# Performance work log

Hardware: AMD Instinct MI355X
Metric: run time of the kernel (lower is better)

Reference implementation:

```python
import jax, jax.numpy as jnp
import numpy as np

S = 2        # scale
KUP = 5      # k_up
EPS = 1e-5   # BatchNorm eps


def _conv(x, w, p):
    return jax.lax.conv_general_dilated(
        x, w, (1, 1), [(p, p), (p, p)],
        dimension_numbers=('NCHW', 'OIHW', 'NCHW'))


def _bn(x, g, b, m, v):
    sc = g * jax.lax.rsqrt(v + EPS)
    return x * sc[None, :, None, None] + (b - m * sc)[None, :, None, None]


def setup_inputs() -> dict:
    key = jax.random.key(0)
    ks = jax.random.split(key, 11)
    c, c_mid = 256, 64
    return {
        'X': jax.random.normal(ks[0], (2, c, 48, 48), jnp.float32),
        'w_comp': jax.random.normal(ks[1], (c_mid, c, 1, 1), jnp.float32) * 0.05,
        'g1': jax.random.uniform(ks[2], (c_mid,), jnp.float32, 0.5, 1.5),
        'b1': jax.random.normal(ks[3], (c_mid,), jnp.float32) * 0.1,
        'm1': jax.random.normal(ks[4], (c_mid,), jnp.float32) * 0.1,
        'v1': jax.random.uniform(ks[5], (c_mid,), jnp.float32, 0.5, 1.5),
        'w_enc': jax.random.normal(ks[6], (100, c_mid, 3, 3), jnp.float32) * 0.05,
        'g2': jax.random.uniform(ks[7], (100,), jnp.float32, 0.5, 1.5),
        'b2': jax.random.normal(ks[8], (100,), jnp.float32) * 0.1,
        'm2': jax.random.normal(ks[9], (100,), jnp.float32) * 0.1,
        'v2': jax.random.uniform(ks[10], (100,), jnp.float32, 0.5, 1.5),
    }


def reference(X, w_comp, g1, b1, m1, v1, w_enc, g2, b2, m2, v2):
    b, c, h, w = X.shape
    h_, w_ = h * S, w * S
    k2 = KUP * KUP
    # comp: 1x1 conv + BN + SiLU
    t = _bn(_conv(X, w_comp, 0), g1, b1, m1, v1)
    t = t * jax.nn.sigmoid(t)
    # enc: 3x3 conv + BN (no act) -> (b, (S*KUP)^2, h, w)
    e = _bn(_conv(t, w_enc, 1), g2, b2, m2, v2)
    # PixelShuffle(S): (b, k2*S*S, h, w) -> (b, k2, h*S, w*S)
    e = e.reshape(b, k2, S, S, h, w).transpose(0, 1, 4, 2, 5, 3).reshape(b, k2, h_, w_)
    Wk = jax.nn.softmax(e, axis=1)  # per-pixel reassembly weights over k_up^2 taps
    # nearest-neighbor upsample by S
    Xup = jnp.repeat(jnp.repeat(X, S, axis=2), S, axis=3)
    # Unfold(kernel=KUP, dilation=S, padding=(KUP//2)*S): spatial size preserved
    pad = (KUP // 2) * S
    xp = jnp.pad(Xup, ((0, 0), (0, 0), (pad, pad), (pad, pad)))
    # taps in row-major (ky, kx) order, matching torch Unfold + view(b,c,k2,h_,w_)
    patches = jnp.stack(
        [xp[:, :, i * S:i * S + h_, j * S:j * S + w_]
         for i in range(KUP) for j in range(KUP)], axis=2)  # (b, c, k2, h_, w_)
    return jnp.einsum('bkhw,bckhw->bchw', Wk, patches)
```

## Files before the change

### kernel.cpp

```cpp
#include <hip/hip_runtime.h>

#define EPS_BN 1e-5f

typedef __attribute__((ext_vector_type(8))) short short8v;
typedef __attribute__((ext_vector_type(4))) float f32x4;
typedef __attribute__((ext_vector_type(4))) _Float16 h16x4;

__device__ inline unsigned short f2bf(float f) {
    union { float f; unsigned u; } v; v.f = f;
    unsigned r = v.u + 0x7fffu + ((v.u >> 16) & 1u);
    return (unsigned short)(r >> 16);
}

__global__ __launch_bounds__(256) void comp_mfma(
    const float* __restrict__ X, const float* __restrict__ w_comp,
    const float* __restrict__ w_enc,
    const float* __restrict__ g1, const float* __restrict__ b1,
    const float* __restrict__ m1, const float* __restrict__ v1,
    unsigned short* __restrict__ tpad, unsigned short* __restrict__ Web)
{
    const int wseg = blockIdx.x;
    const int h = blockIdx.y;
    const int b = blockIdx.z;
    const int tid  = threadIdx.x;

    {
        const int i = ((wseg + 3*(h + 48*b)) << 8) | tid;
        const int ch = i / 576;
        const int r  = i - ch * 576;
        const int kk = r >> 6;
        const int ci = r & 63;
        const float v = (ch < 100) ? w_enc[ch * 576 + ci * 9 + kk] : 0.f;
        Web[i] = f2bf(v);
        if (i < 25088) {
            const int bb  = i / 12544;
            const int rem = i - bb * 12544;
            const int p   = rem >> 6;
            const int chn = rem & 63;
            int rr, cc;
            if (p < 50)       { rr = 0;       cc = p;       }
            else if (p < 100) { rr = 49;      cc = p - 50;  }
            else if (p < 148) { rr = p - 99;  cc = 0;       }
            else              { rr = p - 147; cc = 49;      }
            tpad[((bb*50 + rr)*50 + cc)*64 + chn] = 0;
        }
    }

    const int wave = tid >> 6;
    const int l    = tid & 63;
    const int lr   = l & 15;
    const int lk   = l >> 4;
    const int w0   = wseg * 16;

    const float* xb = X + (size_t)b * 589824 + h * 48 + w0 + lr;
    const float* wb = w_comp + (wave * 16 + lr) * 256;

    float xpre[64];
    #pragma unroll
    for (int s = 0; s < 8; ++s)
        #pragma unroll
        for (int j = 0; j < 8; ++j)
            xpre[s*8 + j] = xb[(size_t)(s*32 + lk*8 + j) * 2304];

    f32x4 acc = {0.f,0.f,0.f,0.f};
    #pragma unroll
    for (int s = 0; s < 8; ++s) {
        const int ci0 = s * 32 + lk * 8;
        short8v a, f;
        const float4 wv0 = *(const float4*)(wb + ci0);
        const float4 wv1 = *(const float4*)(wb + ci0 + 4);
        f[0] = (short)f2bf(wv0.x); f[1] = (short)f2bf(wv0.y);
        f[2] = (short)f2bf(wv0.z); f[3] = (short)f2bf(wv0.w);
        f[4] = (short)f2bf(wv1.x); f[5] = (short)f2bf(wv1.y);
        f[6] = (short)f2bf(wv1.z); f[7] = (short)f2bf(wv1.w);
        #pragma unroll
        for (int j = 0; j < 8; ++j)
            a[j] = (short)f2bf(xpre[s*8 + j]);
        acc = __builtin_amdgcn_mfma_f32_16x16x32_bf16(a, f, acc, 0, 0, 0);
    }

    const int oc = wave * 16 + lr;
    const float sc = g1[oc] * rsqrtf(v1[oc] + EPS_BN);
    const float sh = b1[oc] - m1[oc] * sc;
    unsigned short* tp = tpad + ((b*50 + h + 1)*50 + 1)*64 + oc;
    #pragma unroll
    for (int r = 0; r < 4; ++r) {
        float v = fmaf(acc[r], sc, sh);
        float t = v / (1.f + __expf(-v));
        tp[(w0 + lk*4 + r)*64] = f2bf(t);
    }
}

__global__ __launch_bounds__(256) void enc_sm(
    const unsigned short* __restrict__ tpad, const unsigned short* __restrict__ Web,
    const float* __restrict__ g2, const float* __restrict__ b2,
    const float* __restrict__ m2, const float* __restrict__ v2,
    _Float16* __restrict__ Wl)
{
    const int wseg = blockIdx.x;
    const int h = blockIdx.y;
    const int b = blockIdx.z;
    const int tid  = threadIdx.x;
    const int wave = tid >> 6;
    const int l    = tid & 63;
    const int lr   = l & 15;
    const int lk   = l >> 4;
    const int w0   = wseg * 16;
    const int nt0  = wave * 2, nt1 = wave * 2 + 1;
    __shared__ float elds[16 * 116];

    f32x4 acc0 = {0.f,0.f,0.f,0.f};
    f32x4 acc1 = {0.f,0.f,0.f,0.f};

    const unsigned short* tb = tpad + (b*50 + h)*50*64;
    const unsigned short* wb0 = Web + (nt0*16 + lr)*576;
    const unsigned short* wb1 = Web + (nt1*16 + lr)*576;

    #pragma unroll 6
    for (int s = 0; s < 18; ++s) {
        const int kk = s >> 1;
        const int ky = (kk * 11) >> 5;
        const int kx = kk - ky * 3;
        const int cio = ((s & 1) << 5) + lk * 8;
        const short8v a  = *(const short8v*)(tb + (ky*50 + w0 + kx + lr)*64 + cio);
        const short8v f0 = *(const short8v*)(wb0 + kk*64 + cio);
        const short8v f1 = *(const short8v*)(wb1 + kk*64 + cio);
        acc0 = __builtin_amdgcn_mfma_f32_16x16x32_bf16(a, f0, acc0, 0, 0, 0);
        acc1 = __builtin_amdgcn_mfma_f32_16x16x32_bf16(a, f1, acc1, 0, 0, 0);
    }

    #pragma unroll
    for (int t = 0; t < 2; ++t) {
        const int nt = t ? nt1 : nt0;
        if (nt >= 7) continue;
        const int ch = nt*16 + lr;
        float sc = 0.f, sh = 0.f;
        if (ch < 100) {
            sc = g2[ch] * rsqrtf(v2[ch] + EPS_BN);
            sh = b2[ch] - m2[ch]*sc;
        }
        const f32x4 acc = t ? acc1 : acc0;
        #pragma unroll
        for (int r = 0; r < 4; ++r)
            elds[(lk*4 + r)*116 + ch] = fmaf(acc[r], sc, sh);
    }
    __syncthreads();

    if (tid < 64) {
        const int px = tid >> 2;
        const int s  = tid & 3;
        const float* ep = &elds[px*116 + s];
        float ev[25];
        float mx = -1e30f;
        #pragma unroll
        for (int k = 0; k < 25; ++k) { ev[k] = ep[4*k]; mx = fmaxf(mx, ev[k]); }
        float sum = 0.f;
        #pragma unroll
        for (int k = 0; k < 25; ++k) { ev[k] = __expf(ev[k] - mx); sum += ev[k]; }
        const float rs = 1.f / sum;
        _Float16* wp = Wl + ((b*48 + h)*48 + w0 + px)*112 + s*28;
        #pragma unroll
        for (int k4 = 0; k4 < 6; ++k4) {
            h16x4 o = { (_Float16)(ev[k4*4+0]*rs), (_Float16)(ev[k4*4+1]*rs),
                        (_Float16)(ev[k4*4+2]*rs), (_Float16)(ev[k4*4+3]*rs) };
            *(h16x4*)(wp + k4*4) = o;
        }
        wp[24] = (_Float16)(ev[24]*rs);
    }
}

__global__ __launch_bounds__(256) void carafe_v10(
    const float* __restrict__ X, const _Float16* __restrict__ Wl,
    float* __restrict__ out)
{
    const int bid  = blockIdx.x;
    const int slot = bid & 7;
    const int k    = bid >> 3;
    const int h    = slot + 8 * (k % 6);
    const int cg   = (k / 6) & 15;
    const int b    = k / 96;

    __shared__ float xl[4240];
    __shared__ float ol[3072];
    const int tid = threadIdx.x;

    for (int idx = tid; idx < 960; idx += 256) {
        const int ci  = idx / 60;
        const int rem = idx - ci * 60;
        const int r   = rem / 12;
        const int q   = rem - r * 12;
        const int hh  = h - 2 + r;
        float4 v = {0.f,0.f,0.f,0.f};
        if ((unsigned)hh < 48u)
            v = *(const float4*)&X[(size_t)(b*256 + cg*16 + ci)*2304 + hh*48 + q*4];
        float* base = &xl[(((ci>>2)*5 + r)*53 + 2 + q*4)*4 + (ci&3)];
        base[0]  = v.x;
        base[4]  = v.y;
        base[8]  = v.z;
        base[12] = v.w;
    }
    for (int idx = tid; idx < 320; idx += 256) {
        const int ci  = idx / 20;
        const int rem = idx - ci * 20;
        const int r   = rem / 4;
        const int e   = rem & 3;
        const int cp  = (e < 2) ? e : 48 + e;
        xl[(((ci>>2)*5 + r)*53 + cp)*4 + (ci&3)] = 0.f;
    }
    __syncthreads();

    const int c4g = tid & 3;
    const int w   = tid >> 2;
    if (w < 48) {
        float4 xv[25];
        #pragma unroll
        for (int r = 0; r < 5; ++r)
            #pragma unroll
            for (int dx = 0; dx < 5; ++dx)
                xv[r*5 + dx] = *(const float4*)&xl[((c4g*5 + r)*53 + (w + dx))*4];
        const _Float16* wb = &Wl[(size_t)((b*48 + h)*48 + w)*112];
        #pragma unroll
        for (int s = 0; s < 4; ++s) {
            float ax=0.f, ay=0.f, az=0.f, aw=0.f;
            #pragma unroll
            for (int k4 = 0; k4 < 6; ++k4) {
                const h16x4 hv = *(const h16x4*)&wb[s*28 + k4*4];
                const float w0f = (float)hv[0], w1f = (float)hv[1];
                const float w2f = (float)hv[2], w3f = (float)hv[3];
                const float4 p0 = xv[k4*4+0], p1 = xv[k4*4+1], p2 = xv[k4*4+2], p3 = xv[k4*4+3];
                ax = fmaf(w0f,p0.x,fmaf(w1f,p1.x,fmaf(w2f,p2.x,fmaf(w3f,p3.x,ax))));
                ay = fmaf(w0f,p0.y,fmaf(w1f,p1.y,fmaf(w2f,p2.y,fmaf(w3f,p3.y,ay))));
                az = fmaf(w0f,p0.z,fmaf(w1f,p1.z,fmaf(w2f,p2.z,fmaf(w3f,p3.z,az))));
                aw = fmaf(w0f,p0.w,fmaf(w1f,p1.w,fmaf(w2f,p2.w,fmaf(w3f,p3.w,aw))));
            }
            const float wk = (float)wb[s*28 + 24];
            const float4 pl = xv[24];
            ax = fmaf(wk,pl.x,ax); ay = fmaf(wk,pl.y,ay);
            az = fmaf(wk,pl.z,az); aw = fmaf(wk,pl.w,aw);
            const int y = s >> 1;
            const int x = 2*w + (s & 1);
            ol[((c4g*4 + 0)*2 + y)*96 + x] = ax;
            ol[((c4g*4 + 1)*2 + y)*96 + x] = ay;
            ol[((c4g*4 + 2)*2 + y)*96 + x] = az;
            ol[((c4g*4 + 3)*2 + y)*96 + x] = aw;
        }
    }
    __syncthreads();

    #pragma unroll
    for (int p = 0; p < 3; ++p) {
        const int fi = p*256 + tid;
        const int ch = fi / 48;
        const int rem = fi - ch*48;
        const int y  = rem / 24;
        const int xq = rem - y*24;
        const float4 v = *(const float4*)&ol[fi*4];
        *(float4*)&out[((size_t)(b*256 + cg*16 + ch)*96 + 2*h + y)*96 + xq*4] = v;
    }
}

extern "C" void kernel_launch(void* const* d_in, const int* in_sizes, int n_in,
                              void* d_out, int out_size, void* d_ws, size_t ws_size,
                              hipStream_t stream)
{
    (void)in_sizes; (void)n_in; (void)out_size; (void)ws_size;
    const float* X      = (const float*)d_in[0];
    const float* w_comp = (const float*)d_in[1];
    const float* g1     = (const float*)d_in[2];
    const float* b1     = (const float*)d_in[3];
    const float* m1     = (const float*)d_in[4];
    const float* v1     = (const float*)d_in[5];
    const float* w_enc  = (const float*)d_in[6];
    const float* g2     = (const float*)d_in[7];
    const float* b2     = (const float*)d_in[8];
    const float* m2     = (const float*)d_in[9];
    const float* v2     = (const float*)d_in[10];
    float* out = (float*)d_out;

    char* ws = (char*)d_ws;
    unsigned short* tpad = (unsigned short*)(ws + 0);
    unsigned short* Web  = (unsigned short*)(ws + 640000);
    _Float16*       Wl   = (_Float16*)(ws + 787456);

    dim3 gA(3, 48, 2);
    comp_mfma<<<gA, 256, 0, stream>>>(X, w_comp, w_enc, g1, b1, m1, v1, tpad, Web);
    dim3 gB(3, 48, 2);
    enc_sm<<<gB, 256, 0, stream>>>(tpad, Web, g2, b2, m2, v2, Wl);
    carafe_v10<<<1536, 256, 0, stream>>>(X, Wl, out);
}
```

Measured before the change: 38.52 us.

## Fuse 1x1 comp conv and 3x3 enc conv into one kernel via LDS halo tile

Merges the compression conv and the encoder conv into a single kernel. Each block recomputes the 1x1 conv plus SiLU on a 3x18 halo tile, stored in swizzled shared memory, and then runs the 3x3 conv straight from LDS. This drops one launch and the global round trip through the padded intermediate. The costs are recomputing halo pixels (54 vs 16 per block) and converting enc weights from fp32 with strided gathers inside the MFMA loop instead of reading a prepacked bf16 buffer.

```diff
diff --git a/kernel.cpp b/kernel.cpp
--- a/kernel.cpp
+++ b/kernel.cpp
@@ -12,87 +12,11 @@
     return (unsigned short)(r >> 16);
 }
 
-__global__ __launch_bounds__(256) void comp_mfma(
+__global__ __launch_bounds__(256) void fused_front(
     const float* __restrict__ X, const float* __restrict__ w_comp,
     const float* __restrict__ w_enc,
     const float* __restrict__ g1, const float* __restrict__ b1,
     const float* __restrict__ m1, const float* __restrict__ v1,
-    unsigned short* __restrict__ tpad, unsigned short* __restrict__ Web)
-{
-    const int wseg = blockIdx.x;
-    const int h = blockIdx.y;
-    const int b = blockIdx.z;
-    const int tid  = threadIdx.x;
-
-    {
-        const int i = ((wseg + 3*(h + 48*b)) << 8) | tid;
-        const int ch = i / 576;
-        const int r  = i - ch * 576;
-        const int kk = r >> 6;
-        const int ci = r & 63;
-        const float v = (ch < 100) ? w_enc[ch * 576 + ci * 9 + kk] : 0.f;
-        Web[i] = f2bf(v);
-        if (i < 25088) {
-            const int bb  = i / 12544;
-            const int rem = i - bb * 12544;
-            const int p   = rem >> 6;
-            const int chn = rem & 63;
-            int rr, cc;
-            if (p < 50)       { rr = 0;       cc = p;       }
-            else if (p < 100) { rr = 49;      cc = p - 50;  }
-            else if (p < 148) { rr = p - 99;  cc = 0;       }
-            else              { rr = p - 147; cc = 49;      }
-            tpad[((bb*50 + rr)*50 + cc)*64 + chn] = 0;
-        }
-    }
-
-    const int wave = tid >> 6;
-    const int l    = tid & 63;
-    const int lr   = l & 15;
-    const int lk   = l >> 4;
-    const int w0   = wseg * 16;
-
-    const float* xb = X + (size_t)b * 589824 + h * 48 + w0 + lr;
-    const float* wb = w_comp + (wave * 16 + lr) * 256;
-
-    float xpre[64];
-    #pragma unroll
-    for (int s = 0; s < 8; ++s)
-        #pragma unroll
-        for (int j = 0; j < 8; ++j)
-            xpre[s*8 + j] = xb[(size_t)(s*32 + lk*8 + j) * 2304];
-
-    f32x4 acc = {0.f,0.f,0.f,0.f};
-    #pragma unroll
-    for (int s = 0; s < 8; ++s) {
-        const int ci0 = s * 32 + lk * 8;
-        short8v a, f;
-        const float4 wv0 = *(const float4*)(wb + ci0);
-        const float4 wv1 = *(const float4*)(wb + ci0 + 4);
-        f[0] = (short)f2bf(wv0.x); f[1] = (short)f2bf(wv0.y);
-        f[2] = (short)f2bf(wv0.z); f[3] = (short)f2bf(wv0.w);
-        f[4] = (short)f2bf(wv1.x); f[5] = (short)f2bf(wv1.y);
-        f[6] = (short)f2bf(wv1.z); f[7] = (short)f2bf(wv1.w);
-        #pragma unroll
-        for (int j = 0; j < 8; ++j)
-            a[j] = (short)f2bf(xpre[s*8 + j]);
-        acc = __builtin_amdgcn_mfma_f32_16x16x32_bf16(a, f, acc, 0, 0, 0);
-    }
-
-    const int oc = wave * 16 + lr;
-    const float sc = g1[oc] * rsqrtf(v1[oc] + EPS_BN);
-    const float sh = b1[oc] - m1[oc] * sc;
-    unsigned short* tp = tpad + ((b*50 + h + 1)*50 + 1)*64 + oc;
-    #pragma unroll
-    for (int r = 0; r < 4; ++r) {
-        float v = fmaf(acc[r], sc, sh);
-        float t = v / (1.f + __expf(-v));
-        tp[(w0 + lk*4 + r)*64] = f2bf(t);
-    }
-}
-
-__global__ __launch_bounds__(256) void enc_sm(
-    const unsigned short* __restrict__ tpad, const unsigned short* __restrict__ Web,
     const float* __restrict__ g2, const float* __restrict__ b2,
     const float* __restrict__ m2, const float* __restrict__ v2,
     _Float16* __restrict__ Wl)
@@ -106,43 +30,119 @@
     const int lr   = l & 15;
     const int lk   = l >> 4;
     const int w0   = wseg * 16;
-    const int nt0  = wave * 2, nt1 = wave * 2 + 1;
+
+    __shared__ unsigned short tl[56 * 64];
     __shared__ float elds[16 * 116];
 
-    f32x4 acc0 = {0.f,0.f,0.f,0.f};
-    f32x4 acc1 = {0.f,0.f,0.f,0.f};
-
-    const unsigned short* tb = tpad + (b*50 + h)*50*64;
-    const unsigned short* wb0 = Web + (nt0*16 + lr)*576;
-    const unsigned short* wb1 = Web + (nt1*16 + lr)*576;
-
-    #pragma unroll 6
-    for (int s = 0; s < 18; ++s) {
-        const int kk = s >> 1;
-        const int ky = (kk * 11) >> 5;
-        const int kx = kk - ky * 3;
-        const int cio = ((s & 1) << 5) + lk * 8;
-        const short8v a  = *(const short8v*)(tb + (ky*50 + w0 + kx + lr)*64 + cio);
-        const short8v f0 = *(const short8v*)(wb0 + kk*64 + cio);
-        const short8v f1 = *(const short8v*)(wb1 + kk*64 + cio);
-        acc0 = __builtin_amdgcn_mfma_f32_16x16x32_bf16(a, f0, acc0, 0, 0, 0);
-        acc1 = __builtin_amdgcn_mfma_f32_16x16x32_bf16(a, f1, acc1, 0, 0, 0);
-    }
-
-    #pragma unroll
-    for (int t = 0; t < 2; ++t) {
-        const int nt = t ? nt1 : nt0;
-        if (nt >= 7) continue;
-        const int ch = nt*16 + lr;
-        float sc = 0.f, sh = 0.f;
-        if (ch < 100) {
-            sc = g2[ch] * rsqrtf(v2[ch] + EPS_BN);
-            sh = b2[ch] - m2[ch]*sc;
-        }
-        const f32x4 acc = t ? acc1 : acc0;
-        #pragma unroll
-        for (int r = 0; r < 4; ++r)
-            elds[(lk*4 + r)*116 + ch] = fmaf(acc[r], sc, sh);
+    {
+        const int px  = wave * 16 + lr;
+        const int row = px / 18;
+        const int col = px - row * 18;
+        const int hg  = h - 1 + row;
+        const int wg  = w0 - 1 + col;
+        const bool av = (px < 54) && ((unsigned)hg < 48u) && ((unsigned)wg < 48u);
+        const float* xb = X + (size_t)b * 589824 + hg * 48 + wg;
+
+        float xpre[64];
+        if (av) {
+            #pragma unroll
+            for (int s = 0; s < 8; ++s)
+                #pragma unroll
+                for (int j = 0; j < 8; ++j)
+                    xpre[s*8 + j] = xb[(size_t)(s*32 + lk*8 + j) * 2304];
+        } else {
+            #pragma unroll
+            for (int i = 0; i < 64; ++i) xpre[i] = 0.f;
+        }
+
+        const float* wb = w_comp + lr * 256;
+        f32x4 acc[4] = {{0,0,0,0},{0,0,0,0},{0,0,0,0},{0,0,0,0}};
+        #pragma unroll
+        for (int s = 0; s < 8; ++s) {
+            const int ci0 = s * 32 + lk * 8;
+            short8v a;
+            #pragma unroll
+            for (int j = 0; j < 8; ++j)
+                a[j] = (short)f2bf(xpre[s*8 + j]);
+            #pragma unroll
+            for (int nt = 0; nt < 4; ++nt) {
+                const float4 wv0 = *(const float4*)(wb + nt*4096 + ci0);
+                const float4 wv1 = *(const float4*)(wb + nt*4096 + ci0 + 4);
+                short8v f;
+                f[0] = (short)f2bf(wv0.x); f[1] = (short)f2bf(wv0.y);
+                f[2] = (short)f2bf(wv0.z); f[3] = (short)f2bf(wv0.w);
+                f[4] = (short)f2bf(wv1.x); f[5] = (short)f2bf(wv1.y);
+                f[6] = (short)f2bf(wv1.z); f[7] = (short)f2bf(wv1.w);
+                acc[nt] = __builtin_amdgcn_mfma_f32_16x16x32_bf16(a, f, acc[nt], 0, 0, 0);
+            }
+        }
+        #pragma unroll
+        for (int nt = 0; nt < 4; ++nt) {
+            const int oc = nt * 16 + lr;
+            const float sc = g1[oc] * rsqrtf(v1[oc] + EPS_BN);
+            const float sh = b1[oc] - m1[oc] * sc;
+            #pragma unroll
+            for (int r = 0; r < 4; ++r) {
+                const int pxo = wave * 16 + lk * 4 + r;
+                if (pxo < 54) {
+                    const int prow = pxo / 18;
+                    const int pcol = pxo - prow * 18;
+                    const int phg  = h - 1 + prow;
+                    const int pwg  = w0 - 1 + pcol;
+                    const bool inimg = ((unsigned)phg < 48u) && ((unsigned)pwg < 48u);
+                    float v = fmaf(acc[nt][r], sc, sh);
+                    float t = v / (1.f + __expf(-v));
+                    const int byte = (pxo * 128 + oc * 2) ^ ((pxo & 7) << 4);
+                    *(unsigned short*)((char*)tl + byte) = inimg ? f2bf(t) : (unsigned short)0;
+                }
+            }
+        }
+    }
+    __syncthreads();
+
+    {
+        const int nt0 = wave * 2, nt1 = wave * 2 + 1;
+        const int ch0 = nt0*16 + lr;
+        const int ch1 = nt1*16 + lr;
+        f32x4 acc0 = {0.f,0.f,0.f,0.f};
+        f32x4 acc1 = {0.f,0.f,0.f,0.f};
+        const float* we0 = w_enc + ch0 * 576;
+        const float* we1 = w_enc + ch1 * 576;
+
+        #pragma unroll 6
+        for (int s = 0; s < 18; ++s) {
+            const int kk = s >> 1;
+            const int ky = (kk * 11) >> 5;
+            const int kx = kk - ky * 3;
+            const int cio = ((s & 1) << 5) + lk * 8;
+            const int pa  = ky * 18 + lr + kx;
+            const int byte = (pa * 128 + cio * 2) ^ ((pa & 7) << 4);
+            const short8v a = *(const short8v*)((char*)tl + byte);
+            short8v f0, f1;
+            #pragma unroll
+            for (int j = 0; j < 8; ++j) {
+                f0[j] = (ch0 < 100) ? (short)f2bf(we0[(cio + j)*9 + kk]) : (short)0;
+                f1[j] = (ch1 < 100) ? (short)f2bf(we1[(cio + j)*9 + kk]) : (short)0;
+            }
+            acc0 = __builtin_amdgcn_mfma_f32_16x16x32_bf16(a, f0, acc0, 0, 0, 0);
+            acc1 = __builtin_amdgcn_mfma_f32_16x16x32_bf16(a, f1, acc1, 0, 0, 0);
+        }
+
+        #pragma unroll
+        for (int t = 0; t < 2; ++t) {
+            const int nt = t ? nt1 : nt0;
+            if (nt >= 7) continue;
+            const int ch = nt*16 + lr;
+            float sc = 0.f, sh = 0.f;
+            if (ch < 100) {
+                sc = g2[ch] * rsqrtf(v2[ch] + EPS_BN);
+                sh = b2[ch] - m2[ch]*sc;
+            }
+            const f32x4 acc = t ? acc1 : acc0;
+            #pragma unroll
+            for (int r = 0; r < 4; ++r)
+                elds[(lk*4 + r)*116 + ch] = fmaf(acc[r], sc, sh);
+        }
     }
     __syncthreads();
 
@@ -277,14 +277,10 @@
     const float* v2     = (const float*)d_in[10];
     float* out = (float*)d_out;
 
-    char* ws = (char*)d_ws;
-    unsigned short* tpad = (unsigned short*)(ws + 0);
-    unsigned short* Web  = (unsigned short*)(ws + 640000);
-    _Float16*       Wl   = (_Float16*)(ws + 787456);
-
-    dim3 gA(3, 48, 2);
-    comp_mfma<<<gA, 256, 0, stream>>>(X, w_comp, w_enc, g1, b1, m1, v1, tpad, Web);
-    dim3 gB(3, 48, 2);
-    enc_sm<<<gB, 256, 0, stream>>>(tpad, Web, g2, b2, m2, v2, Wl);
+    _Float16* Wl = (_Float16*)d_ws;
+
+    dim3 gF(3, 48, 2);
+    fused_front<<<gF, 256, 0, stream>>>(X, w_comp, w_enc, g1, b1, m1, v1,
+                                        g2, b2, m2, v2, Wl);
     carafe_v10<<<1536, 256, 0, stream>>>(X, Wl, out);
 }
```

Result: slower. 117.2 us (+204.2%).
